# Optimization experiments

Measured on AMD Instinct MI355X. Metric: run time of the kernel, lower is better.

Reference implementation:

```python
import jax, jax.numpy as jnp
import numpy as np

B, H, LQ, LK, D = 2, 16, 2048, 2048, 128

def setup_inputs() -> dict:
    key = jax.random.key(0)
    k1, k2, k3 = jax.random.split(key, 3)
    q = jax.random.normal(k1, (B, H, LQ, D), dtype=jnp.float32)
    k = jax.random.normal(k2, (B, H, LK, D), dtype=jnp.float32)
    v = jax.random.normal(k3, (B, H, LK, D), dtype=jnp.float32)
    return {"q": q, "k": k, "v": v}

def reference(q, k, v):
    # scaled dot-product attention: softmax(q k^T / sqrt(D)) v
    scale = q.shape[-1] ** (-0.5)
    # scores: [B,H,Lq,Lk]
    scores = jnp.einsum('bhqd,bhkd->bhqk', q, k) * scale
    attn = jax.nn.softmax(scores, axis=-1)
    out = jnp.einsum('bhqk,bhkd->bhqd', attn, v)  # [B,H,Lq,Dv]
    return out
```

## Files before the change

### kernel.cpp

```cpp
#include <hip/hip_runtime.h>
#include <hip/hip_bf16.h>
#include <cstdint>

#define LQ_N   2048
#define LK_N   2048
#define DD     128
#define NHEADS 32
#define QBLK   128
#define KVBLK  64
#define NKV    (LK_N / KVBLK)
#define NQB    (LQ_N / QBLK)
#define SCALE  0.08838834764831845f
#define SCALE2 0.1275525003267101f

#define KTILE_BYTES (KVBLK * DD * 2)
#define WS_K_BYTES  ((size_t)NHEADS * NKV * KTILE_BYTES)
#define WS_NEED     (2 * WS_K_BYTES)

#define PSTR 72

typedef __attribute__((ext_vector_type(8)))  short bf16x8;
typedef __attribute__((ext_vector_type(4)))  float f32x4;
typedef __attribute__((ext_vector_type(16))) float f32x16;

#if __has_builtin(__builtin_amdgcn_exp2f)
#define EXP2F __builtin_amdgcn_exp2f
#else
#define EXP2F exp2f
#endif

__device__ inline unsigned short f2bf(float f) {
    union { float f; unsigned u; } x; x.f = f;
    unsigned r = (x.u + 0x7fffu + ((x.u >> 16) & 1u)) >> 16;
    return (unsigned short)r;
}

__device__ inline unsigned cvt_pk_bf16(float lo, float hi) {
    unsigned r;
    asm("v_cvt_pk_bf16_f32 %0, %1, %2" : "=v"(r) : "v"(lo), "v"(hi));
    return r;
}

__device__ inline bf16x8 make_pfrag(float v0, float v1, float v2, float v3,
                                    float v4, float v5, float v6, float v7) {
    unsigned a0 = cvt_pk_bf16(v0, v1);
    unsigned a1 = cvt_pk_bf16(v2, v3);
    unsigned b0 = cvt_pk_bf16(v4, v5);
    unsigned b1 = cvt_pk_bf16(v6, v7);
    asm volatile("v_permlane32_swap_b32 %0, %1" : "+v"(a0), "+v"(b0));
    asm volatile("v_permlane32_swap_b32 %0, %1" : "+v"(a1), "+v"(b1));
    union { unsigned u[4]; bf16x8 v8; } u;
    u.u[0] = a0; u.u[1] = a1; u.u[2] = b0; u.u[3] = b1;
    return u.v8;
}

__device__ inline void gld16(const char* g, const char* l) {
    __builtin_amdgcn_global_load_lds(
        (const __attribute__((address_space(1))) unsigned int*)g,
        (__attribute__((address_space(3))) unsigned int*)l,
        16, 0, 0);
}

__global__ __launch_bounds__(256, 2)
void prep_k_kernel(const float* __restrict__ K, char* __restrict__ ws)
{
    __shared__ unsigned short kt[KVBLK * 136];
    const int tid  = threadIdx.x;
    const int kvt  = blockIdx.x;
    const int head = blockIdx.y;
    const float* Kh = K + ((size_t)head * LK_N + (size_t)kvt * KVBLK) * DD;
    #pragma unroll
    for (int i = 0; i < 4; ++i) {
        int c = tid + 256 * i;
        int r  = c >> 4;
        int c8 = c & 15;
        const float* src = Kh + (size_t)r * DD + c8 * 8;
        float4 a = *(const float4*)src;
        float4 b = *(const float4*)(src + 4);
        bf16x8 t;
        t[0] = (short)f2bf(a.x * SCALE2); t[1] = (short)f2bf(a.y * SCALE2);
        t[2] = (short)f2bf(a.z * SCALE2); t[3] = (short)f2bf(a.w * SCALE2);
        t[4] = (short)f2bf(b.x * SCALE2); t[5] = (short)f2bf(b.y * SCALE2);
        t[6] = (short)f2bf(b.z * SCALE2); t[7] = (short)f2bf(b.w * SCALE2);
        *(bf16x8*)&kt[r * 136 + c8 * 8] = t;
    }
    __syncthreads();
    char* dst = ws + ((size_t)head * NKV + kvt) * KTILE_BYTES;
    #pragma unroll
    for (int i = 0; i < 4; ++i) {
        int c = tid + 256 * i;
        int g = c >> 6;
        int r = c & 63;
        bf16x8 t = *(const bf16x8*)&kt[r * 136 + g * 8];
        *(bf16x8*)(dst + c * 16) = t;
    }
}

__global__ __launch_bounds__(256, 2)
void prep_vt_kernel(const float* __restrict__ V, char* __restrict__ ws)
{
    __shared__ unsigned short vt[DD * PSTR];
    const int tid  = threadIdx.x;
    const int kvt  = blockIdx.x;
    const int head = blockIdx.y;
    const float* Vh = V + ((size_t)head * LK_N + (size_t)kvt * KVBLK) * DD;
    #pragma unroll
    for (int i = 0; i < 8; ++i) {
        int f = tid + 256 * i;
        int r  = f >> 5;
        int c4 = f & 31;
        float4 x = *(const float4*)(Vh + (size_t)r * DD + c4 * 4);
        vt[(c4 * 4 + 0) * PSTR + r] = f2bf(x.x);
        vt[(c4 * 4 + 1) * PSTR + r] = f2bf(x.y);
        vt[(c4 * 4 + 2) * PSTR + r] = f2bf(x.z);
        vt[(c4 * 4 + 3) * PSTR + r] = f2bf(x.w);
    }
    __syncthreads();
    char* dst = ws + WS_K_BYTES + ((size_t)head * NKV + kvt) * KTILE_BYTES;
    #pragma unroll
    for (int i = 0; i < 4; ++i) {
        int c = tid + 256 * i;
        int g = c >> 7;
        int d = c & 127;
        bf16x8 t = *(const bf16x8*)&vt[d * PSTR + g * 8];
        *(bf16x8*)(dst + c * 16) = t;
    }
}

__global__ __launch_bounds__(256, 2)
void attn_main_kernel(const float* __restrict__ Q, const char* __restrict__ kws,
                      const char* __restrict__ vws, float* __restrict__ O)
{
    __shared__ unsigned short kt_lds[2][KVBLK * DD];
    __shared__ unsigned short vt_lds[2][DD * KVBLK];

    const int tid  = threadIdx.x;
    const int lane = tid & 63;
    const int wave = tid >> 6;
    const int l31  = lane & 31;
    const int h    = lane >> 5;

    const int bid  = blockIdx.x;
    const int sid  = (bid & 7) * (NQB * NHEADS / 8) + (bid >> 3);
    const int head = sid >> 4;
    const int qb   = sid & 15;

    const float* Qh = Q + (size_t)head * LQ_N * DD;
    float*       Oh = O + (size_t)head * LQ_N * DD;
    const char*  kt_g = kws + (size_t)head * NKV * KTILE_BYTES;
    const char*  vt_g = vws + (size_t)head * NKV * KTILE_BYTES;

    const int qrow = qb * QBLK + wave * 32 + l31;
    bf16x8 qf[8];
    {
        const float* qp = Qh + (size_t)qrow * DD + 8 * h;
        #pragma unroll
        for (int kd = 0; kd < 8; ++kd) {
            float4 a = *(const float4*)(qp + 16 * kd);
            float4 b = *(const float4*)(qp + 16 * kd + 4);
            bf16x8 t;
            t[0] = (short)f2bf(a.x); t[1] = (short)f2bf(a.y);
            t[2] = (short)f2bf(a.z); t[3] = (short)f2bf(a.w);
            t[4] = (short)f2bf(b.x); t[5] = (short)f2bf(b.y);
            t[6] = (short)f2bf(b.z); t[7] = (short)f2bf(b.w);
            qf[kd] = t;
        }
    }
    asm volatile("s_waitcnt vmcnt(0)" ::: "memory");

    f32x16 o_acc[4];
    #pragma unroll
    for (int nt = 0; nt < 4; ++nt)
        #pragma unroll
        for (int i = 0; i < 16; ++i) o_acc[nt][i] = 0.f;
    float m_run = -1e30f, l_run = 0.f;

    auto issue = [&](int t, int b) {
        const char* ks = kt_g + (size_t)t * KTILE_BYTES;
        const char* vs = vt_g + (size_t)t * KTILE_BYTES;
        const char* kl = (const char*)&kt_lds[b][0];
        const char* vl = (const char*)&vt_lds[b][0];
        #pragma unroll
        for (int i = 0; i < 4; ++i) {
            int off = (tid + 256 * i) * 16;
            gld16(ks + off, kl + off);
            gld16(vs + off, vl + off);
        }
    };
    issue(0, 0);
    issue(1, 1);

    for (int t = 0; t < NKV; ++t) {
        if (t < NKV - 1) asm volatile("s_waitcnt vmcnt(8)" ::: "memory");
        else             asm volatile("s_waitcnt vmcnt(0)" ::: "memory");
        __builtin_amdgcn_s_barrier();

        const char* kb = (const char*)&kt_lds[t & 1][0];
        const char* vb = (const char*)&vt_lds[t & 1][0];

        f32x16 s0, s1;
        #pragma unroll
        for (int i = 0; i < 16; ++i) { s0[i] = 0.f; s1[i] = 0.f; }
        __builtin_amdgcn_s_setprio(1);
        #pragma unroll
        for (int kd = 0; kd < 8; ++kd) {
            int g = 2 * kd + h;
            bf16x8 kf0 = *(const bf16x8*)(kb + ((g * 64 + l31) << 4));
            bf16x8 kf1 = *(const bf16x8*)(kb + ((g * 64 + 32 + l31) << 4));
            s0 = __builtin_amdgcn_mfma_f32_32x32x16_bf16(kf0, qf[kd], s0, 0, 0, 0);
            s1 = __builtin_amdgcn_mfma_f32_32x32x16_bf16(kf1, qf[kd], s1, 0, 0, 0);
        }
        __builtin_amdgcn_s_setprio(0);

        float pmax = s0[0];
        #pragma unroll
        for (int i = 1; i < 16; ++i) pmax = fmaxf(pmax, s0[i]);
        #pragma unroll
        for (int i = 0; i < 16; ++i) pmax = fmaxf(pmax, s1[i]);
        pmax = fmaxf(pmax, __shfl_xor(pmax, 32));

        if (!__all(pmax <= m_run + 8.0f)) {
            float mn = fmaxf(m_run, pmax);
            float al = EXP2F(m_run - mn);
            m_run = mn;
            l_run *= al;
            #pragma unroll
            for (int nt = 0; nt < 4; ++nt)
                #pragma unroll
                for (int i = 0; i < 16; ++i) o_acc[nt][i] *= al;
        }
        float sum = 0.f;
        #pragma unroll
        for (int i = 0; i < 16; ++i) { s0[i] = EXP2F(s0[i] - m_run); sum += s0[i]; }
        #pragma unroll
        for (int i = 0; i < 16; ++i) { s1[i] = EXP2F(s1[i] - m_run); sum += s1[i]; }
        sum += __shfl_xor(sum, 32);
        l_run += sum;

        bf16x8 pf0 = make_pfrag(s0[0], s0[1], s0[2],  s0[3],  s0[4],  s0[5],  s0[6],  s0[7]);
        bf16x8 pf1 = make_pfrag(s0[8], s0[9], s0[10], s0[11], s0[12], s0[13], s0[14], s0[15]);
        bf16x8 pf2 = make_pfrag(s1[0], s1[1], s1[2],  s1[3],  s1[4],  s1[5],  s1[6],  s1[7]);
        bf16x8 pf3 = make_pfrag(s1[8], s1[9], s1[10], s1[11], s1[12], s1[13], s1[14], s1[15]);

        __builtin_amdgcn_s_setprio(1);
        #pragma unroll
        for (int nt = 0; nt < 4; ++nt) {
            int d = 32 * nt + l31;
            bf16x8 vf0 = *(const bf16x8*)(vb + (((0 + h) * 128 + d) << 4));
            bf16x8 vf1 = *(const bf16x8*)(vb + (((2 + h) * 128 + d) << 4));
            bf16x8 vf2 = *(const bf16x8*)(vb + (((4 + h) * 128 + d) << 4));
            bf16x8 vf3 = *(const bf16x8*)(vb + (((6 + h) * 128 + d) << 4));
            o_acc[nt] = __builtin_amdgcn_mfma_f32_32x32x16_bf16(vf0, pf0, o_acc[nt], 0, 0, 0);
            o_acc[nt] = __builtin_amdgcn_mfma_f32_32x32x16_bf16(vf1, pf1, o_acc[nt], 0, 0, 0);
            o_acc[nt] = __builtin_amdgcn_mfma_f32_32x32x16_bf16(vf2, pf2, o_acc[nt], 0, 0, 0);
            o_acc[nt] = __builtin_amdgcn_mfma_f32_32x32x16_bf16(vf3, pf3, o_acc[nt], 0, 0, 0);
        }
        __builtin_amdgcn_s_setprio(0);

        __builtin_amdgcn_s_barrier();
        if (t + 2 < NKV) issue(t + 2, t & 1);
    }

    float inv = 1.0f / l_run;
    float* op = Oh + (size_t)qrow * DD;
    #pragma unroll
    for (int nt = 0; nt < 4; ++nt)
        #pragma unroll
        for (int p = 0; p < 4; ++p) {
            int dbase = 32 * nt + 8 * p + 4 * h;
            float4 w;
            w.x = o_acc[nt][4 * p + 0] * inv;
            w.y = o_acc[nt][4 * p + 1] * inv;
            w.z = o_acc[nt][4 * p + 2] * inv;
            w.w = o_acc[nt][4 * p + 3] * inv;
            *(float4*)(op + dbase) = w;
        }
}

#define KSTRIDE  136
#define VTSTRIDE 40
#define FKV 32

__global__ __launch_bounds__(256, 2)
void attn_fwd_fallback(const float* __restrict__ Q, const float* __restrict__ K,
                       const float* __restrict__ V, float* __restrict__ O)
{
    __shared__ unsigned short k_lds[FKV * KSTRIDE];
    __shared__ unsigned short vt_lds[DD * VTSTRIDE];
    __shared__ unsigned short p_lds2[4 * 16 * VTSTRIDE];

    const int tid  = threadIdx.x;
    const int lane = tid & 63;
    const int wave = tid >> 6;
    const int head = blockIdx.y;
    const int qb   = blockIdx.x;

    const float* Qh = Q + (size_t)head * LQ_N * DD;
    const float* Kh = K + (size_t)head * LK_N * DD;
    const float* Vh = V + (size_t)head * LK_N * DD;
    float*       Oh = O + (size_t)head * LQ_N * DD;

    const int r16 = lane & 15;
    const int g   = lane >> 4;

    const int qrow = qb * 64 + wave * 16 + r16;
    bf16x8 qf[4];
    {
        const float* qp = Qh + (size_t)qrow * DD + 8 * g;
        #pragma unroll
        for (int kt = 0; kt < 4; ++kt) {
            float4 a = *(const float4*)(qp + 32 * kt);
            float4 b = *(const float4*)(qp + 32 * kt + 4);
            bf16x8 t;
            t[0] = (short)f2bf(a.x * SCALE); t[1] = (short)f2bf(a.y * SCALE);
            t[2] = (short)f2bf(a.z * SCALE); t[3] = (short)f2bf(a.w * SCALE);
            t[4] = (short)f2bf(b.x * SCALE); t[5] = (short)f2bf(b.y * SCALE);
            t[6] = (short)f2bf(b.z * SCALE); t[7] = (short)f2bf(b.w * SCALE);
            qf[kt] = t;
        }
    }

    f32x4 o_acc[8];
    #pragma unroll
    for (int dt = 0; dt < 8; ++dt) o_acc[dt] = (f32x4){0.f, 0.f, 0.f, 0.f};
    float m_run[4], l_run[4];
    #pragma unroll
    for (int r = 0; r < 4; ++r) { m_run[r] = -1e30f; l_run[r] = 0.f; }

    for (int kv = 0; kv < LK_N / FKV; ++kv) {
        const float* Kt = Kh + (size_t)kv * FKV * DD;
        const float* Vt = Vh + (size_t)kv * FKV * DD;
        __syncthreads();
        #pragma unroll
        for (int i = 0; i < 4; ++i) {
            int f = tid + 256 * i;
            int row = f >> 5, colf = f & 31;
            float4 x = *(const float4*)(Kt + (size_t)row * DD + colf * 4);
            ushort4 pk;
            pk.x = f2bf(x.x); pk.y = f2bf(x.y); pk.z = f2bf(x.z); pk.w = f2bf(x.w);
            *(ushort4*)(&k_lds[row * KSTRIDE + colf * 4]) = pk;
        }
        #pragma unroll
        for (int i = 0; i < 4; ++i) {
            int f = tid + 256 * i;
            int row = f >> 5, colf = f & 31;
            float4 x = *(const float4*)(Vt + (size_t)row * DD + colf * 4);
            vt_lds[(colf * 4 + 0) * VTSTRIDE + row] = f2bf(x.x);
            vt_lds[(colf * 4 + 1) * VTSTRIDE + row] = f2bf(x.y);
            vt_lds[(colf * 4 + 2) * VTSTRIDE + row] = f2bf(x.z);
            vt_lds[(colf * 4 + 3) * VTSTRIDE + row] = f2bf(x.w);
        }
        __syncthreads();

        f32x4 s0 = (f32x4){0.f,0.f,0.f,0.f};
        f32x4 s1 = (f32x4){0.f,0.f,0.f,0.f};
        #pragma unroll
        for (int kt = 0; kt < 4; ++kt) {
            bf16x8 kf0 = *(const bf16x8*)&k_lds[(r16)      * KSTRIDE + 32 * kt + 8 * g];
            bf16x8 kf1 = *(const bf16x8*)&k_lds[(16 + r16) * KSTRIDE + 32 * kt + 8 * g];
            s0 = __builtin_amdgcn_mfma_f32_16x16x32_bf16(qf[kt], kf0, s0, 0, 0, 0);
            s1 = __builtin_amdgcn_mfma_f32_16x16x32_bf16(qf[kt], kf1, s1, 0, 0, 0);
        }

        float alpha[4];
        f32x4 p0, p1;
        #pragma unroll
        for (int r = 0; r < 4; ++r) {
            float t = fmaxf(s0[r], s1[r]);
            t = fmaxf(t, __shfl_xor(t, 1));
            t = fmaxf(t, __shfl_xor(t, 2));
            t = fmaxf(t, __shfl_xor(t, 4));
            t = fmaxf(t, __shfl_xor(t, 8));
            float mn = fmaxf(m_run[r], t);
            alpha[r] = __expf(m_run[r] - mn);
            m_run[r] = mn;
            p0[r] = __expf(s0[r] - mn);
            p1[r] = __expf(s1[r] - mn);
            float su = p0[r] + p1[r];
            su += __shfl_xor(su, 1);
            su += __shfl_xor(su, 2);
            su += __shfl_xor(su, 4);
            su += __shfl_xor(su, 8);
            l_run[r] = l_run[r] * alpha[r] + su;
        }

        unsigned short* pw = &p_lds2[wave * 16 * VTSTRIDE];
        #pragma unroll
        for (int r = 0; r < 4; ++r) {
            int row = 4 * g + r;
            pw[row * VTSTRIDE + r16]      = f2bf(p0[r]);
            pw[row * VTSTRIDE + 16 + r16] = f2bf(p1[r]);
        }
        bf16x8 pf = *(const bf16x8*)&pw[r16 * VTSTRIDE + 8 * g];

        #pragma unroll
        for (int dt = 0; dt < 8; ++dt) {
            #pragma unroll
            for (int r = 0; r < 4; ++r) o_acc[dt][r] *= alpha[r];
        }
        #pragma unroll
        for (int dt = 0; dt < 8; ++dt) {
            bf16x8 vf = *(const bf16x8*)&vt_lds[(16 * dt + r16) * VTSTRIDE + 8 * g];
            o_acc[dt] = __builtin_amdgcn_mfma_f32_16x16x32_bf16(pf, vf, o_acc[dt], 0, 0, 0);
        }
    }

    #pragma unroll
    for (int r = 0; r < 4; ++r) {
        float inv = 1.0f / l_run[r];
        int row = qb * 64 + wave * 16 + 4 * g + r;
        float* op = Oh + (size_t)row * DD + r16;
        #pragma unroll
        for (int dt = 0; dt < 8; ++dt)
            op[16 * dt] = o_acc[dt][r] * inv;
    }
}

extern "C" void kernel_launch(void* const* d_in, const int* in_sizes, int n_in,
                              void* d_out, int out_size, void* d_ws, size_t ws_size,
                              hipStream_t stream) {
    const float* q = (const float*)d_in[0];
    const float* k = (const float*)d_in[1];
    const float* v = (const float*)d_in[2];
    float* o = (float*)d_out;

    if (ws_size >= WS_NEED) {
        char* ws = (char*)d_ws;
        prep_k_kernel <<<dim3(NKV, NHEADS), 256, 0, stream>>>(k, ws);
        prep_vt_kernel<<<dim3(NKV, NHEADS), 256, 0, stream>>>(v, ws);
        attn_main_kernel<<<dim3(NQB * NHEADS), 256, 0, stream>>>(
            q, ws, ws + WS_K_BYTES, o);
    } else {
        attn_fwd_fallback<<<dim3(LQ_N / 64, NHEADS), 256, 0, stream>>>(q, k, v, o);
    }
}
```

Baseline: 101.1 us.

## Software-pipeline QK^T of next tile with softmax+PV of previous tile

Restructures the main attention loop so the QK^T MFMAs for tile t+1 are issued before the softmax and PV work for tile t, using two sets of score registers. K keeps double buffering while V moves to triple buffering in dynamic shared memory (5 tiles, 80 KB), so V tiles stay resident one step longer. The aim is to overlap the softmax VALU work with matrix-core work and hide LDS and global latency. In exchange it holds more registers live and uses more LDS per block, which may cut occupancy below the requested two blocks per CU. It also adds a hipFuncSetAttribute call on every launch.

```diff
diff --git a/kernel.cpp b/kernel.cpp
--- a/kernel.cpp
+++ b/kernel.cpp
@@ -16,6 +16,10 @@
 #define KTILE_BYTES (KVBLK * DD * 2)
 #define WS_K_BYTES  ((size_t)NHEADS * NKV * KTILE_BYTES)
 #define WS_NEED     (2 * WS_K_BYTES)
+
+#define KB_OFF(b)   ((b) * KTILE_BYTES)
+#define VB_OFF(s)   (2 * KTILE_BYTES + (s) * KTILE_BYTES)
+#define SMEM_MAIN   (5 * KTILE_BYTES)
 
 #define PSTR 72
 
@@ -131,8 +135,7 @@
 void attn_main_kernel(const float* __restrict__ Q, const char* __restrict__ kws,
                       const char* __restrict__ vws, float* __restrict__ O)
 {
-    __shared__ unsigned short kt_lds[2][KVBLK * DD];
-    __shared__ unsigned short vt_lds[2][DD * KVBLK];
+    extern __shared__ char smem[];
 
     const int tid  = threadIdx.x;
     const int lane = tid & 63;
@@ -175,11 +178,11 @@
         for (int i = 0; i < 16; ++i) o_acc[nt][i] = 0.f;
     float m_run = -1e30f, l_run = 0.f;
 
-    auto issue = [&](int t, int b) {
+    auto issue = [&](int t) {
         const char* ks = kt_g + (size_t)t * KTILE_BYTES;
         const char* vs = vt_g + (size_t)t * KTILE_BYTES;
-        const char* kl = (const char*)&kt_lds[b][0];
-        const char* vl = (const char*)&vt_lds[b][0];
+        const char* kl = smem + KB_OFF(t & 1);
+        const char* vl = smem + VB_OFF(t % 3);
         #pragma unroll
         for (int i = 0; i < 4; ++i) {
             int off = (tid + 256 * i) * 16;
@@ -187,18 +190,8 @@
             gld16(vs + off, vl + off);
         }
     };
-    issue(0, 0);
-    issue(1, 1);
-
-    for (int t = 0; t < NKV; ++t) {
-        if (t < NKV - 1) asm volatile("s_waitcnt vmcnt(8)" ::: "memory");
-        else             asm volatile("s_waitcnt vmcnt(0)" ::: "memory");
-        __builtin_amdgcn_s_barrier();
-
-        const char* kb = (const char*)&kt_lds[t & 1][0];
-        const char* vb = (const char*)&vt_lds[t & 1][0];
-
-        f32x16 s0, s1;
+
+    auto do_qk = [&](f32x16& s0, f32x16& s1, const char* kb) {
         #pragma unroll
         for (int i = 0; i < 16; ++i) { s0[i] = 0.f; s1[i] = 0.f; }
         __builtin_amdgcn_s_setprio(1);
@@ -211,7 +204,9 @@
             s1 = __builtin_amdgcn_mfma_f32_32x32x16_bf16(kf1, qf[kd], s1, 0, 0, 0);
         }
         __builtin_amdgcn_s_setprio(0);
-
+    };
+
+    auto do_smpv = [&](f32x16& s0, f32x16& s1, const char* vb) {
         float pmax = s0[0];
         #pragma unroll
         for (int i = 1; i < 16; ++i) pmax = fmaxf(pmax, s0[i]);
@@ -256,10 +251,40 @@
             o_acc[nt] = __builtin_amdgcn_mfma_f32_32x32x16_bf16(vf3, pf3, o_acc[nt], 0, 0, 0);
         }
         __builtin_amdgcn_s_setprio(0);
-
+    };
+
+    f32x16 sA0, sA1, sB0, sB1;
+
+    issue(0);
+    issue(1);
+
+    asm volatile("s_waitcnt vmcnt(8)" ::: "memory");
+    __builtin_amdgcn_s_barrier();
+    do_qk(sA0, sA1, smem + KB_OFF(0));
+    __builtin_amdgcn_s_barrier();
+    issue(2);
+
+    for (int t = 1; t < NKV - 1; t += 2) {
+        asm volatile("s_waitcnt vmcnt(8)" ::: "memory");
         __builtin_amdgcn_s_barrier();
-        if (t + 2 < NKV) issue(t + 2, t & 1);
-    }
+        do_qk(sB0, sB1, smem + KB_OFF(1));
+        do_smpv(sA0, sA1, smem + VB_OFF((t - 1) % 3));
+        __builtin_amdgcn_s_barrier();
+        issue(t + 2);
+
+        asm volatile("s_waitcnt vmcnt(8)" ::: "memory");
+        __builtin_amdgcn_s_barrier();
+        do_qk(sA0, sA1, smem + KB_OFF(0));
+        do_smpv(sB0, sB1, smem + VB_OFF(t % 3));
+        __builtin_amdgcn_s_barrier();
+        if (t + 3 < NKV) issue(t + 3);
+    }
+
+    asm volatile("s_waitcnt vmcnt(0)" ::: "memory");
+    __builtin_amdgcn_s_barrier();
+    do_qk(sB0, sB1, smem + KB_OFF(1));
+    do_smpv(sA0, sA1, smem + VB_OFF((NKV - 2) % 3));
+    do_smpv(sB0, sB1, smem + VB_OFF((NKV - 1) % 3));
 
     float inv = 1.0f / l_run;
     float* op = Oh + (size_t)qrow * DD;
@@ -424,11 +449,15 @@
     const float* v = (const float*)d_in[2];
     float* o = (float*)d_out;
 
-    if (ws_size >= WS_NEED) {
+    hipError_t attr_ok = hipFuncSetAttribute(
+        (const void*)attn_main_kernel,
+        hipFuncAttributeMaxDynamicSharedMemorySize, SMEM_MAIN);
+
+    if (ws_size >= WS_NEED && attr_ok == hipSuccess) {
         char* ws = (char*)d_ws;
         prep_k_kernel <<<dim3(NKV, NHEADS), 256, 0, stream>>>(k, ws);
         prep_vt_kernel<<<dim3(NKV, NHEADS), 256, 0, stream>>>(v, ws);
-        attn_main_kernel<<<dim3(NQB * NHEADS), 256, 0, stream>>>(
+        attn_main_kernel<<<dim3(NQB * NHEADS), 256, SMEM_MAIN, stream>>>(
             q, ws, ws + WS_K_BYTES, o);
     } else {
         attn_fwd_fallback<<<dim3(LQ_N / 64, NHEADS), 256, 0, stream>>>(q, k, v, o);
```

Result: no change. 100.8 us (-0.4%).

## Load V fragments directly from global into registers, keep only K in LDS

Applied to the files above, without the earlier changes.

V tiles are no longer staged through LDS. Each wave loads its V fragments straight from global memory into 16 registers at the start of each iteration, while K stays double-buffered in LDS. The exp/convert step is interleaved with the PV MFMAs per 8-element chunk, the max reduction becomes a tree, and the setprio hints are dropped. This halves LDS traffic and footprint, but adds register pressure, exposes global load latency for V inside the loop, and relies on a hand-tuned vmcnt(20) wait.

```diff
diff --git a/kernel.cpp b/kernel.cpp
--- a/kernel.cpp
+++ b/kernel.cpp
@@ -29,6 +29,8 @@
 #define EXP2F exp2f
 #endif
 
+#define MFMA32(a, b, c) __builtin_amdgcn_mfma_f32_32x32x16_bf16((a), (b), (c), 0, 0, 0)
+
 __device__ inline unsigned short f2bf(float f) {
     union { float f; unsigned u; } x; x.f = f;
     unsigned r = (x.u + 0x7fffu + ((x.u >> 16) & 1u)) >> 16;
@@ -39,6 +41,10 @@
     unsigned r;
     asm("v_cvt_pk_bf16_f32 %0, %1, %2" : "=v"(r) : "v"(lo), "v"(hi));
     return r;
+}
+
+__device__ inline float fmax4(float a, float b, float c, float d) {
+    return fmaxf(fmaxf(a, b), fmaxf(c, d));
 }
 
 __device__ inline bf16x8 make_pfrag(float v0, float v1, float v2, float v3,
@@ -47,8 +53,8 @@
     unsigned a1 = cvt_pk_bf16(v2, v3);
     unsigned b0 = cvt_pk_bf16(v4, v5);
     unsigned b1 = cvt_pk_bf16(v6, v7);
-    asm volatile("v_permlane32_swap_b32 %0, %1" : "+v"(a0), "+v"(b0));
-    asm volatile("v_permlane32_swap_b32 %0, %1" : "+v"(a1), "+v"(b1));
+    asm("v_permlane32_swap_b32 %0, %1" : "+v"(a0), "+v"(b0));
+    asm("v_permlane32_swap_b32 %0, %1" : "+v"(a1), "+v"(b1));
     union { unsigned u[4]; bf16x8 v8; } u;
     u.u[0] = a0; u.u[1] = a1; u.u[2] = b0; u.u[3] = b1;
     return u.v8;
@@ -131,8 +137,7 @@
 void attn_main_kernel(const float* __restrict__ Q, const char* __restrict__ kws,
                       const char* __restrict__ vws, float* __restrict__ O)
 {
-    __shared__ unsigned short kt_lds[2][KVBLK * DD];
-    __shared__ unsigned short vt_lds[2][DD * KVBLK];
+    __shared__ bf16x8 kbuf[2][KTILE_BYTES / 16];
 
     const int tid  = threadIdx.x;
     const int lane = tid & 63;
@@ -175,52 +180,61 @@
         for (int i = 0; i < 16; ++i) o_acc[nt][i] = 0.f;
     float m_run = -1e30f, l_run = 0.f;
 
-    auto issue = [&](int t, int b) {
+    auto issue_k = [&](int t) {
         const char* ks = kt_g + (size_t)t * KTILE_BYTES;
-        const char* vs = vt_g + (size_t)t * KTILE_BYTES;
-        const char* kl = (const char*)&kt_lds[b][0];
-        const char* vl = (const char*)&vt_lds[b][0];
+        const char* kl = (const char*)&kbuf[t & 1][0];
         #pragma unroll
         for (int i = 0; i < 4; ++i) {
             int off = (tid + 256 * i) * 16;
             gld16(ks + off, kl + off);
-            gld16(vs + off, vl + off);
         }
     };
-    issue(0, 0);
-    issue(1, 1);
+
+    issue_k(0);
+    issue_k(1);
 
     for (int t = 0; t < NKV; ++t) {
-        if (t < NKV - 1) asm volatile("s_waitcnt vmcnt(8)" ::: "memory");
-        else             asm volatile("s_waitcnt vmcnt(0)" ::: "memory");
+        bf16x8 vr[16];
+        {
+            const char* vtile = vt_g + (size_t)t * KTILE_BYTES;
+            #pragma unroll
+            for (int ks = 0; ks < 4; ++ks)
+                #pragma unroll
+                for (int nt = 0; nt < 4; ++nt)
+                    vr[4 * ks + nt] = *(const bf16x8*)
+                        (vtile + (((2 * ks + h) * 128 + 32 * nt + l31) << 4));
+        }
+
+        asm volatile("s_waitcnt vmcnt(20)" ::: "memory");
         __builtin_amdgcn_s_barrier();
 
-        const char* kb = (const char*)&kt_lds[t & 1][0];
-        const char* vb = (const char*)&vt_lds[t & 1][0];
+        const char* kb = (const char*)&kbuf[t & 1][0];
 
         f32x16 s0, s1;
         #pragma unroll
         for (int i = 0; i < 16; ++i) { s0[i] = 0.f; s1[i] = 0.f; }
-        __builtin_amdgcn_s_setprio(1);
         #pragma unroll
         for (int kd = 0; kd < 8; ++kd) {
-            int g = 2 * kd + h;
-            bf16x8 kf0 = *(const bf16x8*)(kb + ((g * 64 + l31) << 4));
-            bf16x8 kf1 = *(const bf16x8*)(kb + ((g * 64 + 32 + l31) << 4));
-            s0 = __builtin_amdgcn_mfma_f32_32x32x16_bf16(kf0, qf[kd], s0, 0, 0, 0);
-            s1 = __builtin_amdgcn_mfma_f32_32x32x16_bf16(kf1, qf[kd], s1, 0, 0, 0);
-        }
-        __builtin_amdgcn_s_setprio(0);
-
-        float pmax = s0[0];
-        #pragma unroll
-        for (int i = 1; i < 16; ++i) pmax = fmaxf(pmax, s0[i]);
-        #pragma unroll
-        for (int i = 0; i < 16; ++i) pmax = fmaxf(pmax, s1[i]);
-        pmax = fmaxf(pmax, __shfl_xor(pmax, 32));
-
-        if (!__all(pmax <= m_run + 8.0f)) {
-            float mn = fmaxf(m_run, pmax);
+            bf16x8 kf0 = *(const bf16x8*)(kb + (((2 * kd + h) * 64 + l31) << 4));
+            bf16x8 kf1 = *(const bf16x8*)(kb + (((2 * kd + h) * 64 + 32 + l31) << 4));
+            s0 = MFMA32(kf0, qf[kd], s0);
+            s1 = MFMA32(kf1, qf[kd], s1);
+        }
+
+        float x0 = fmax4(s0[0],  s0[1],  s0[2],  s0[3]);
+        float x1 = fmax4(s0[4],  s0[5],  s0[6],  s0[7]);
+        float x2 = fmax4(s0[8],  s0[9],  s0[10], s0[11]);
+        float x3 = fmax4(s0[12], s0[13], s0[14], s0[15]);
+        float y0 = fmax4(s1[0],  s1[1],  s1[2],  s1[3]);
+        float y1 = fmax4(s1[4],  s1[5],  s1[6],  s1[7]);
+        float y2 = fmax4(s1[8],  s1[9],  s1[10], s1[11]);
+        float y3 = fmax4(s1[12], s1[13], s1[14], s1[15]);
+        float pm = fmaxf(fmaxf(fmaxf(x0, x1), fmaxf(x2, x3)),
+                         fmaxf(fmaxf(y0, y1), fmaxf(y2, y3)));
+        pm = fmaxf(pm, __shfl_xor(pm, 32));
+
+        if (!__all(pm <= m_run + 8.0f)) {
+            float mn = fmaxf(m_run, pm);
             float al = EXP2F(m_run - mn);
             m_run = mn;
             l_run *= al;
@@ -229,36 +243,34 @@
                 #pragma unroll
                 for (int i = 0; i < 16; ++i) o_acc[nt][i] *= al;
         }
+
         float sum = 0.f;
         #pragma unroll
-        for (int i = 0; i < 16; ++i) { s0[i] = EXP2F(s0[i] - m_run); sum += s0[i]; }
-        #pragma unroll
-        for (int i = 0; i < 16; ++i) { s1[i] = EXP2F(s1[i] - m_run); sum += s1[i]; }
+        for (int half = 0; half < 2; ++half) {
+            f32x16& S = half ? s1 : s0;
+            #pragma unroll
+            for (int sub = 0; sub < 2; ++sub) {
+                const int B = sub * 8;
+                const int KS = half * 2 + sub;
+                float e0 = EXP2F(S[B + 0] - m_run), e1 = EXP2F(S[B + 1] - m_run);
+                float e2 = EXP2F(S[B + 2] - m_run), e3 = EXP2F(S[B + 3] - m_run);
+                float e4 = EXP2F(S[B + 4] - m_run), e5 = EXP2F(S[B + 5] - m_run);
+                float e6 = EXP2F(S[B + 6] - m_run), e7 = EXP2F(S[B + 7] - m_run);
+                sum += ((e0 + e1) + (e2 + e3)) + ((e4 + e5) + (e6 + e7));
+                bf16x8 pf = make_pfrag(e0, e1, e2, e3, e4, e5, e6, e7);
+                o_acc[0] = MFMA32(vr[4 * KS + 0], pf, o_acc[0]);
+                o_acc[1] = MFMA32(vr[4 * KS + 1], pf, o_acc[1]);
+                o_acc[2] = MFMA32(vr[4 * KS + 2], pf, o_acc[2]);
+                o_acc[3] = MFMA32(vr[4 * KS + 3], pf, o_acc[3]);
+            }
+        }
         sum += __shfl_xor(sum, 32);
         l_run += sum;
 
-        bf16x8 pf0 = make_pfrag(s0[0], s0[1], s0[2],  s0[3],  s0[4],  s0[5],  s0[6],  s0[7]);
-        bf16x8 pf1 = make_pfrag(s0[8], s0[9], s0[10], s0[11], s0[12], s0[13], s0[14], s0[15]);
-        bf16x8 pf2 = make_pfrag(s1[0], s1[1], s1[2],  s1[3],  s1[4],  s1[5],  s1[6],  s1[7]);
-        bf16x8 pf3 = make_pfrag(s1[8], s1[9], s1[10], s1[11], s1[12], s1[13], s1[14], s1[15]);
-
-        __builtin_amdgcn_s_setprio(1);
-        #pragma unroll
-        for (int nt = 0; nt < 4; ++nt) {
-            int d = 32 * nt + l31;
-            bf16x8 vf0 = *(const bf16x8*)(vb + (((0 + h) * 128 + d) << 4));
-            bf16x8 vf1 = *(const bf16x8*)(vb + (((2 + h) * 128 + d) << 4));
-            bf16x8 vf2 = *(const bf16x8*)(vb + (((4 + h) * 128 + d) << 4));
-            bf16x8 vf3 = *(const bf16x8*)(vb + (((6 + h) * 128 + d) << 4));
-            o_acc[nt] = __builtin_amdgcn_mfma_f32_32x32x16_bf16(vf0, pf0, o_acc[nt], 0, 0, 0);
-            o_acc[nt] = __builtin_amdgcn_mfma_f32_32x32x16_bf16(vf1, pf1, o_acc[nt], 0, 0, 0);
-            o_acc[nt] = __builtin_amdgcn_mfma_f32_32x32x16_bf16(vf2, pf2, o_acc[nt], 0, 0, 0);
-            o_acc[nt] = __builtin_amdgcn_mfma_f32_32x32x16_bf16(vf3, pf3, o_acc[nt], 0, 0, 0);
-        }
-        __builtin_amdgcn_s_setprio(0);
-
+        asm volatile("s_waitcnt lgkmcnt(0)" ::: "memory");
+        __builtin_amdgcn_sched_barrier(0);
         __builtin_amdgcn_s_barrier();
-        if (t + 2 < NKV) issue(t + 2, t & 1);
+        if (t + 2 < NKV) issue_k(t + 2);
     }
 
     float inv = 1.0f / l_run;
```

Measured after the change: 103.5 us. 2.3% more time.
